# Optimization experiments

Measured on AMD Instinct MI355X. Metric: run time of the kernel, lower is better.

Reference implementation:

```python
import jax, jax.numpy as jnp
import numpy as np

D_MODEL = 1536
BLOCK = 3
N_BLOCKS = D_MODEL // BLOCK
BATCH = 8192
EPS = 1e-8


def setup_inputs() -> dict:
    key = jax.random.key(0)
    ks = jax.random.split(key, 6)
    s = 1.0 / np.sqrt(D_MODEL)  # torch Linear default-ish scale
    x = jax.random.normal(ks[0], (BATCH, D_MODEL), dtype=jnp.float32)
    h_prev = jax.random.normal(ks[1], (BATCH, D_MODEL), dtype=jnp.float32)
    W_biv = jax.random.normal(ks[2], (D_MODEL, D_MODEL), dtype=jnp.float32) * s
    b_biv = jnp.zeros((D_MODEL,), dtype=jnp.float32)  # init.zeros_
    W_dec = jax.random.normal(ks[3], (1, D_MODEL), dtype=jnp.float32) * s
    b_dec = jnp.full((1,), 1.4, dtype=jnp.float32)  # init.constant_(1.4)
    W_in = jax.random.normal(ks[4], (D_MODEL, D_MODEL), dtype=jnp.float32) * s
    b_in = jax.random.normal(ks[5], (D_MODEL,), dtype=jnp.float32) * s
    return {"x": x, "h_prev": h_prev, "W_biv": W_biv, "b_biv": b_biv,
            "W_dec": W_dec, "b_dec": b_dec, "W_in": W_in, "b_in": b_in}


def _quat_rotate_blocks(h_blocks, bivectors):
    # h_blocks, bivectors: (batch, n_blocks, 3)
    norm_b = jnp.maximum(jnp.linalg.norm(bivectors, axis=-1, keepdims=True), EPS)
    half_angle = norm_b / 2
    w = jnp.cos(half_angle)[..., 0]
    s = (jnp.sin(half_angle) / norm_b)[..., 0]  # sin_ha_over_norm[..., 0]
    # NOTE: faithful to source — qx/qy/qz all use component 0 of sin_ha_over_norm
    qx = s * bivectors[..., 2]
    qy = -s * bivectors[..., 1]
    qz = s * bivectors[..., 0]
    vx, vy, vz = h_blocks[..., 0], h_blocks[..., 1], h_blocks[..., 2]
    tx = 2 * (qy * vz - qz * vy)
    ty = 2 * (qz * vx - qx * vz)
    tz = 2 * (qx * vy - qy * vx)
    rx = vx + w * tx + (qy * tz - qz * ty)
    ry = vy + w * ty + (qz * tx - qx * tz)
    rz = vz + w * tz + (qx * ty - qy * tx)
    return jnp.stack([rx, ry, rz], axis=-1)


def reference(x, h_prev, W_biv, b_biv, W_dec, b_dec, W_in, b_in):
    batch = x.shape[0]
    bivectors = (x @ W_biv.T + b_biv).reshape(batch, N_BLOCKS, 3)
    decay = jax.nn.sigmoid(x @ W_dec.T + b_dec)          # (batch, 1)
    injection = x @ W_in.T + b_in                        # (batch, d_model)
    h_blocks = h_prev.reshape(batch, N_BLOCKS, 3)
    rotated = _quat_rotate_blocks(h_blocks, bivectors)
    return decay * rotated.reshape(batch, D_MODEL) + injection
```

## Files before the change

kernel.cpp:

```cpp
#include <hip/hip_runtime.h>
#include <cstdint>

#define D_MODEL 1536
#define BATCH   8192
#define EPS     1e-8f

#define BM 128
#define BN 96
#define BK 32
#define NT (D_MODEL / BK)
#define NTN (D_MODEL / BN)
#define NTM (BATCH / BM)
#define BUF 20480

typedef __attribute__((ext_vector_type(8))) short bf16x8;
typedef __attribute__((ext_vector_type(8))) unsigned short ushort8;
typedef __attribute__((ext_vector_type(4))) float f32x4;

__device__ __forceinline__ unsigned short f2bf(float f) {
  unsigned u = __builtin_bit_cast(unsigned, f);
  u += 0x7fffu + ((u >> 16) & 1u);
  return (unsigned short)(u >> 16);
}

__device__ __forceinline__ ushort8 pack8u(float4 a, float4 b) {
  ushort8 o;
  o[0] = f2bf(a.x); o[1] = f2bf(a.y); o[2] = f2bf(a.z); o[3] = f2bf(a.w);
  o[4] = f2bf(b.x); o[5] = f2bf(b.y); o[6] = f2bf(b.z); o[7] = f2bf(b.w);
  return o;
}

__device__ __forceinline__ void full_drain() {
  asm volatile("s_waitcnt vmcnt(0) lgkmcnt(0)" ::: "memory");
}
__device__ __forceinline__ void vm_drain() {
  asm volatile("s_waitcnt vmcnt(0)" ::: "memory");
}
__device__ __forceinline__ void lgkm_drain() {
  asm volatile("s_waitcnt lgkmcnt(0)" ::: "memory");
}

__device__ __forceinline__ void load_lds16(const void* g, void* l) {
  __builtin_amdgcn_global_load_lds(
      (const __attribute__((address_space(1))) unsigned int*)g,
      (__attribute__((address_space(3))) unsigned int*)l,
      16, 0, 0);
}

__global__ void prep_all(const float* __restrict__ x,
                         const float* __restrict__ wdec,
                         const float* __restrict__ bdec,
                         const float* __restrict__ wbiv,
                         const float* __restrict__ win,
                         unsigned short* __restrict__ xb,
                         unsigned short* __restrict__ wb,
                         float* __restrict__ decay) {
  const int b = blockIdx.x;
  if (b < 2048) {
    int row  = (int)((b * 256 + threadIdx.x) >> 6);
    int lane = threadIdx.x & 63;
    const float4* xr = (const float4*)(x + (long)row * D_MODEL);
    const float4* wr = (const float4*)wdec;
    unsigned short* xo = xb + (long)row * D_MODEL;
    float acc = 0.f;
#pragma unroll
    for (int i = 0; i < 6; ++i) {
      float4 a = xr[lane + 64 * i];
      float4 w = wr[lane + 64 * i];
      acc += a.x * w.x + a.y * w.y + a.z * w.z + a.w * w.w;
      ushort4 o;
      o.x = f2bf(a.x); o.y = f2bf(a.y); o.z = f2bf(a.z); o.w = f2bf(a.w);
      *(ushort4*)(xo + (lane + 64 * i) * 4) = o;
    }
    for (int off = 32; off; off >>= 1) acc += __shfl_xor(acc, off);
    if (lane == 0) decay[row] = 1.f / (1.f + expf(-(acc + bdec[0])));
  } else {
    const long NW4 = (long)D_MODEL * D_MODEL / 4;
    for (long i = (long)(b - 2048) * 256 + threadIdx.x; i < 2 * NW4;
         i += (long)1024 * 256) {
      const float4* src = (i < NW4) ? (const float4*)wbiv : (const float4*)win;
      long j = (i < NW4) ? i : (i - NW4);
      float4 v = src[j];
      ushort4 o;
      o.x = f2bf(v.x); o.y = f2bf(v.y); o.z = f2bf(v.z); o.w = f2bf(v.w);
      *(ushort4*)(wb + 4 * i) = o;
    }
  }
}

__global__ __launch_bounds__(512, 2)
void fused_main(const unsigned short* __restrict__ xb,
                const unsigned short* __restrict__ wb,
                const float* __restrict__ hprev,
                const float* __restrict__ decay,
                const float* __restrict__ bbiv,
                const float* __restrict__ bin,
                float* __restrict__ out) {
  __shared__ __align__(16) char smem[49664];
  float* sBv = (float*)smem;

  const int bid = blockIdx.x;
  const int tm = bid / NTN, tn = bid % NTN;
  const int m0 = tm * BM, n0 = tn * BN;
  const int tid  = threadIdx.x;
  const int lane = tid & 63, wid = tid >> 6;
  const int wr = wid >> 1, wc = wid & 1;
  const int lr = lane & 15;
  const int lk = lane >> 4;

  const unsigned short *gA, *gB1, *gB2;
  int dA, dB1, dB2;
  {
    int f, row, c, cs;
    f = tid;  row = f >> 2; c = f & 3; cs = c ^ ((row >> 1) & 3);
    gA = xb + (long)(m0 + row) * D_MODEL + cs * 8;
    dA = (wid * 64) << 4;
    row = f >> 2; c = f & 3; cs = c ^ ((row >> 1) & 3);
    gB1 = wb + (long)(n0 + row) * D_MODEL + cs * 8;
    gB2 = gB1 + (long)D_MODEL * D_MODEL;
    dB1 = 8192 + ((wid * 64) << 4);
    dB2 = dB1 + 6144;
  }

  auto STAGE = [&](int bb) {
    load_lds16(gA, smem + bb + dA);
    if (tid < 384) {
      load_lds16(gB1, smem + bb + dB1);
      load_lds16(gB2, smem + bb + dB2);
    }
    gA += BK; gB1 += BK; gB2 += BK;
  };

  f32x4 accB[2][3], accI[2][3];
#pragma unroll
  for (int a = 0; a < 2; ++a)
#pragma unroll
    for (int b = 0; b < 3; ++b) { accB[a][b] = (f32x4)0.f; accI[a][b] = (f32x4)0.f; }

  STAGE(0);
  vm_drain();
  __syncthreads();

  for (int t = 0; t < NT; ++t) {
    const int cur = (t & 1) * BUF;
    if (t + 1 < NT) STAGE(((t + 1) & 1) * BUF);

    const unsigned short* cA  = (const unsigned short*)(smem + cur);
    const unsigned short* cB1 = (const unsigned short*)(smem + cur + 8192);
    const unsigned short* cB2 = (const unsigned short*)(smem + cur + 14336);

    {
      bf16x8 a[2], b1[3], b2[3];
#pragma unroll
      for (int mi = 0; mi < 2; ++mi) {
        int R = wr * 32 + mi * 16 + lr;
        a[mi] = *(const bf16x8*)(cA + R * 32 + (lk ^ ((R >> 1) & 3)) * 8);
      }
#pragma unroll
      for (int ni = 0; ni < 3; ++ni) {
        int R = wc * 48 + ni * 16 + lr;
        b1[ni] = *(const bf16x8*)(cB1 + R * 32 + (lk ^ ((R >> 1) & 3)) * 8);
        b2[ni] = *(const bf16x8*)(cB2 + R * 32 + (lk ^ ((R >> 1) & 3)) * 8);
      }
      lgkm_drain();
      __builtin_amdgcn_sched_barrier(0);
#pragma unroll
      for (int mi = 0; mi < 2; ++mi)
#pragma unroll
        for (int ni = 0; ni < 3; ++ni)
          accB[mi][ni] = __builtin_amdgcn_mfma_f32_16x16x32_bf16(
              a[mi], b1[ni], accB[mi][ni], 0, 0, 0);
      __builtin_amdgcn_sched_barrier(0);
#pragma unroll
      for (int mi = 0; mi < 2; ++mi)
#pragma unroll
        for (int ni = 0; ni < 3; ++ni)
          accI[mi][ni] = __builtin_amdgcn_mfma_f32_16x16x32_bf16(
              a[mi], b2[ni], accI[mi][ni], 0, 0, 0);
      __builtin_amdgcn_sched_barrier(0);
    }

    vm_drain();
    __syncthreads();
  }

#pragma unroll
  for (int mi = 0; mi < 2; ++mi)
#pragma unroll
    for (int ni = 0; ni < 3; ++ni) {
      int col = wc * 48 + ni * 16 + lr;
      float bb = bbiv[n0 + col];
#pragma unroll
      for (int r = 0; r < 4; ++r) {
        int row = wr * 32 + mi * 16 + lk * 4 + r;
        sBv[row * 97 + col] = accB[mi][ni][r] + bb;
      }
    }
  full_drain();
  __syncthreads();

#pragma unroll
  for (int mi = 0; mi < 2; ++mi)
#pragma unroll
    for (int ni = 0; ni < 3; ++ni) {
      int col  = wc * 48 + ni * 16 + lr;
      int gcol = n0 + col;
      int c    = (col % 3);
      int lc0  = col - c;
      float binv = bin[gcol];
#pragma unroll
      for (int r = 0; r < 4; ++r) {
        int row  = wr * 32 + mi * 16 + lk * 4 + r;
        int grow = m0 + row;
        float bx = sBv[row * 97 + lc0];
        float by = sBv[row * 97 + lc0 + 1];
        float bz = sBv[row * 97 + lc0 + 2];
        const float* hp = hprev + (long)grow * D_MODEL + (n0 + lc0);
        float vx = hp[0], vy = hp[1], vz = hp[2];
        float nb = sqrtf(bx * bx + by * by + bz * bz);
        nb = fmaxf(nb, EPS);
        float ha = 0.5f * nb;
        float w  = cosf(ha);
        float s  = sinf(ha) / nb;
        float qx = s * bz, qy = -s * by, qz = s * bx;
        float tx = 2.f * (qy * vz - qz * vy);
        float ty = 2.f * (qz * vx - qx * vz);
        float tz = 2.f * (qx * vy - qy * vx);
        float rx = vx + w * tx + (qy * tz - qz * ty);
        float ry = vy + w * ty + (qz * tx - qx * tz);
        float rz = vz + w * tz + (qx * ty - qy * tx);
        float rc = (c == 0) ? rx : ((c == 1) ? ry : rz);
        out[(long)grow * D_MODEL + gcol] =
            decay[grow] * rc + (accI[mi][ni][r] + binv);
      }
    }
}

__global__ __launch_bounds__(256, 2)
void fused_mfma3(const float* __restrict__ x,
                 const float* __restrict__ wbiv,
                 const float* __restrict__ win,
                 const float* __restrict__ hprev,
                 const float* __restrict__ wdec,
                 const float* __restrict__ bdec,
                 const float* __restrict__ bbiv,
                 const float* __restrict__ bin,
                 float* __restrict__ out) {
  __shared__ __align__(16) char smem[50688];
  __shared__ float sDecay[BM];
  unsigned short* sA  = (unsigned short*)smem;
  unsigned short* sB1 = (unsigned short*)(smem + 16384);
  unsigned short* sB2 = (unsigned short*)(smem + 28672);
  float* sBv = (float*)smem;

  const int bid = blockIdx.x;
  const int tm = bid / NTN, tn = bid % NTN;
  const int m0 = tm * BM, n0 = tn * BN;
  const int tid  = threadIdx.x;
  const int lane = tid & 63, wid = tid >> 6;
  const int wr = wid >> 1, wc = wid & 1;
  const int lr = lane & 15;
  const int lk = lane >> 4;

  {
    const float bd = bdec[0];
    const float4* wd4 = (const float4*)wdec;
    for (int rr = 0; rr < 32; ++rr) {
      int row = wid * 32 + rr;
      const float4* xr = (const float4*)(x + (long)(m0 + row) * D_MODEL);
      float acc = 0.f;
#pragma unroll
      for (int i = 0; i < 6; ++i) {
        float4 a = xr[lane + 64 * i];
        float4 b = wd4[lane + 64 * i];
        acc += a.x * b.x + a.y * b.y + a.z * b.z + a.w * b.w;
      }
      for (int off = 32; off; off >>= 1) acc += __shfl_xor(acc, off);
      if (lane == 0) sDecay[row] = 1.f / (1.f + expf(-(acc + bd)));
    }
  }

  f32x4 accB[4][3], accI[4][3];
#pragma unroll
  for (int a = 0; a < 4; ++a)
#pragma unroll
    for (int b = 0; b < 3; ++b) { accB[a][b] = (f32x4)0.f; accI[a][b] = (f32x4)0.f; }

  for (int kt = 0; kt < D_MODEL; kt += 64) {
    full_drain();
    __syncthreads();
#pragma unroll
    for (int i = 0; i < 4; ++i) {
      int f = i * 256 + tid;
      int row = f >> 3, c = f & 7;
      const float4* p = (const float4*)(x + (long)(m0 + row) * D_MODEL + kt + c * 8);
      *(ushort8*)(sA + row * 64 + c * 8) = pack8u(p[0], p[1]);
    }
#pragma unroll
    for (int i = 0; i < 6; ++i) {
      int mat = (i >= 3);
      int g = (i - 3 * mat) * 256 + tid;
      int row = g >> 3, c = g & 7;
      const float* wsrc = mat ? win : wbiv;
      const float4* p = (const float4*)(wsrc + (long)(n0 + row) * D_MODEL + kt + c * 8);
      *(ushort8*)((mat ? sB2 : sB1) + row * 64 + c * 8) = pack8u(p[0], p[1]);
    }
    full_drain();
    __syncthreads();

#pragma unroll
    for (int ks = 0; ks < 2; ++ks) {
      const int k0 = ks * 32 + lk * 8;
      bf16x8 a[4], b1[3], b2[3];
#pragma unroll
      for (int mi = 0; mi < 4; ++mi)
        a[mi] = *(const bf16x8*)(sA + (wr * 64 + mi * 16 + lr) * 64 + k0);
#pragma unroll
      for (int ni = 0; ni < 3; ++ni) {
        b1[ni] = *(const bf16x8*)(sB1 + (wc * 48 + ni * 16 + lr) * 64 + k0);
        b2[ni] = *(const bf16x8*)(sB2 + (wc * 48 + ni * 16 + lr) * 64 + k0);
      }
      full_drain();
      __builtin_amdgcn_sched_barrier(0);
#pragma unroll
      for (int mi = 0; mi < 4; ++mi)
#pragma unroll
        for (int ni = 0; ni < 3; ++ni)
          accB[mi][ni] = __builtin_amdgcn_mfma_f32_16x16x32_bf16(
              a[mi], b1[ni], accB[mi][ni], 0, 0, 0);
      __builtin_amdgcn_sched_barrier(0);
#pragma unroll
      for (int mi = 0; mi < 4; ++mi)
#pragma unroll
        for (int ni = 0; ni < 3; ++ni)
          accI[mi][ni] = __builtin_amdgcn_mfma_f32_16x16x32_bf16(
              a[mi], b2[ni], accI[mi][ni], 0, 0, 0);
      __builtin_amdgcn_sched_barrier(0);
    }
  }

  full_drain();
  __syncthreads();
#pragma unroll
  for (int mi = 0; mi < 4; ++mi)
#pragma unroll
    for (int ni = 0; ni < 3; ++ni) {
      int col = wc * 48 + ni * 16 + lr;
      float bb = bbiv[n0 + col];
#pragma unroll
      for (int r = 0; r < 4; ++r) {
        int row = wr * 64 + mi * 16 + lk * 4 + r;
        sBv[row * 97 + col] = accB[mi][ni][r] + bb;
      }
    }
  full_drain();
  __syncthreads();

#pragma unroll
  for (int mi = 0; mi < 4; ++mi)
#pragma unroll
    for (int ni = 0; ni < 3; ++ni) {
      int col  = wc * 48 + ni * 16 + lr;
      int gcol = n0 + col;
      int c    = (col % 3);
      int lc0  = col - c;
      float binv = bin[gcol];
#pragma unroll
      for (int r = 0; r < 4; ++r) {
        int row  = wr * 64 + mi * 16 + lk * 4 + r;
        int grow = m0 + row;
        float bx = sBv[row * 97 + lc0];
        float by = sBv[row * 97 + lc0 + 1];
        float bz = sBv[row * 97 + lc0 + 2];
        const float* hp = hprev + (long)grow * D_MODEL + (n0 + lc0);
        float vx = hp[0], vy = hp[1], vz = hp[2];
        float nb = sqrtf(bx * bx + by * by + bz * bz);
        nb = fmaxf(nb, EPS);
        float ha = 0.5f * nb;
        float w  = cosf(ha);
        float s  = sinf(ha) / nb;
        float qx = s * bz, qy = -s * by, qz = s * bx;
        float tx = 2.f * (qy * vz - qz * vy);
        float ty = 2.f * (qz * vx - qx * vz);
        float tz = 2.f * (qx * vy - qy * vx);
        float rx = vx + w * tx + (qy * tz - qz * ty);
        float ry = vy + w * ty + (qz * tx - qx * tz);
        float rz = vz + w * tz + (qx * ty - qy * tx);
        float rc = (c == 0) ? rx : ((c == 1) ? ry : rz);
        out[(long)grow * D_MODEL + gcol] =
            sDecay[row] * rc + (accI[mi][ni][r] + binv);
      }
    }
}

extern "C" void kernel_launch(void* const* d_in, const int* in_sizes, int n_in,
                              void* d_out, int out_size, void* d_ws, size_t ws_size,
                              hipStream_t stream) {
  const float* x     = (const float*)d_in[0];
  const float* hprev = (const float*)d_in[1];
  const float* wbiv  = (const float*)d_in[2];
  const float* bbiv  = (const float*)d_in[3];
  const float* wdec  = (const float*)d_in[4];
  const float* bdec  = (const float*)d_in[5];
  const float* win   = (const float*)d_in[6];
  const float* bin   = (const float*)d_in[7];
  float* out = (float*)d_out;

  const size_t XB_B  = 25165824;
  const size_t WB_B  = 9437184;
  const size_t DC_B  = 32768;

  if (ws_size >= XB_B + WB_B + DC_B) {
    char* ws = (char*)d_ws;
    unsigned short* xb = (unsigned short*)ws;
    unsigned short* wb = (unsigned short*)(ws + XB_B);
    float* decay       = (float*)(ws + XB_B + WB_B);
    prep_all<<<dim3(3072), dim3(256), 0, stream>>>(
        x, wdec, bdec, wbiv, win, xb, wb, decay);
    fused_main<<<dim3(NTM * NTN), dim3(512), 0, stream>>>(
        xb, wb, hprev, decay, bbiv, bin, out);
  } else {
    fused_mfma3<<<dim3(NTM * NTN), dim3(256), 0, stream>>>(
        x, wbiv, win, hprev, wdec, bdec, bbiv, bin, out);
  }
}
```

Before: 134.7 us.

## Double K-tile depth to 64 with 8-way swizzle and use fast sin/cos

Raises the K tile from 32 to 64, so the main loop runs half as many iterations and pays half as many barriers and waits on the global-to-LDS staging. Shared memory per buffer doubles to 40 KB, which can cap occupancy at the declared two blocks of 512 threads. Staging is now a uniform unrolled loop of five async loads per thread with precomputed LDS offsets, using an 8-slot XOR swizzle in place of the old 4-slot one. The epilogue also switches sinf/cosf to the hardware __sinf/__cosf intrinsics, trading some accuracy for fewer instructions.

After: 113.5 us. 1.19x faster.

```diff
diff --git a/kernel.cpp b/kernel.cpp
--- a/kernel.cpp
+++ b/kernel.cpp
@@ -7,11 +7,11 @@
 
 #define BM 128
 #define BN 96
-#define BK 32
+#define BK 64
 #define NT (D_MODEL / BK)
 #define NTN (D_MODEL / BN)
 #define NTM (BATCH / BM)
-#define BUF 20480
+#define BUF 40960
 
 typedef __attribute__((ext_vector_type(8))) short bf16x8;
 typedef __attribute__((ext_vector_type(8))) unsigned short ushort8;
@@ -96,7 +96,7 @@
                 const float* __restrict__ bbiv,
                 const float* __restrict__ bin,
                 float* __restrict__ out) {
-  __shared__ __align__(16) char smem[49664];
+  __shared__ __align__(16) char smem[2 * BUF];
   float* sBv = (float*)smem;
 
   const int bid = blockIdx.x;
@@ -108,28 +108,53 @@
   const int lr = lane & 15;
   const int lk = lane >> 4;
 
-  const unsigned short *gA, *gB1, *gB2;
-  int dA, dB1, dB2;
-  {
-    int f, row, c, cs;
-    f = tid;  row = f >> 2; c = f & 3; cs = c ^ ((row >> 1) & 3);
-    gA = xb + (long)(m0 + row) * D_MODEL + cs * 8;
-    dA = (wid * 64) << 4;
-    row = f >> 2; c = f & 3; cs = c ^ ((row >> 1) & 3);
-    gB1 = wb + (long)(n0 + row) * D_MODEL + cs * 8;
-    gB2 = gB1 + (long)D_MODEL * D_MODEL;
-    dB1 = 8192 + ((wid * 64) << 4);
-    dB2 = dB1 + 6144;
+  const unsigned short* gptr[5];
+  int doff[5];
+#pragma unroll
+  for (int i = 0; i < 5; ++i) {
+    int f = i * 512 + tid;
+    if (f < 1024) {
+      int row = f >> 3, c = f & 7, cs = c ^ (row & 7);
+      gptr[i] = xb + (long)(m0 + row) * D_MODEL + cs * 8;
+      doff[i] = f << 4;
+    } else if (f < 1792) {
+      int g = f - 1024;
+      int row = g >> 3, c = g & 7, cs = c ^ (row & 7);
+      gptr[i] = wb + (long)(n0 + row) * D_MODEL + cs * 8;
+      doff[i] = 16384 + (g << 4);
+    } else {
+      int g = f - 1792;
+      int row = g >> 3, c = g & 7, cs = c ^ (row & 7);
+      gptr[i] = wb + (long)D_MODEL * D_MODEL + (long)(n0 + row) * D_MODEL + cs * 8;
+      doff[i] = 28672 + (g << 4);
+    }
   }
 
   auto STAGE = [&](int bb) {
-    load_lds16(gA, smem + bb + dA);
-    if (tid < 384) {
-      load_lds16(gB1, smem + bb + dB1);
-      load_lds16(gB2, smem + bb + dB2);
-    }
-    gA += BK; gB1 += BK; gB2 += BK;
+#pragma unroll
+    for (int i = 0; i < 5; ++i) {
+      load_lds16(gptr[i], smem + bb + doff[i]);
+      gptr[i] += BK;
+    }
   };
+
+  int offA[2][2], offB1[3][2], offB2[3][2];
+#pragma unroll
+  for (int ks = 0; ks < 2; ++ks) {
+    const int slot = ks * 4 + lk;
+#pragma unroll
+    for (int mi = 0; mi < 2; ++mi) {
+      int R = wr * 32 + mi * 16 + lr;
+      offA[mi][ks] = (R * 64 + (slot ^ (R & 7)) * 8) * 2;
+    }
+#pragma unroll
+    for (int ni = 0; ni < 3; ++ni) {
+      int R = wc * 48 + ni * 16 + lr;
+      int o = (R * 64 + (slot ^ (R & 7)) * 8) * 2;
+      offB1[ni][ks] = 16384 + o;
+      offB2[ni][ks] = 28672 + o;
+    }
+  }
 
   f32x4 accB[2][3], accI[2][3];
 #pragma unroll
@@ -145,22 +170,16 @@
     const int cur = (t & 1) * BUF;
     if (t + 1 < NT) STAGE(((t + 1) & 1) * BUF);
 
-    const unsigned short* cA  = (const unsigned short*)(smem + cur);
-    const unsigned short* cB1 = (const unsigned short*)(smem + cur + 8192);
-    const unsigned short* cB2 = (const unsigned short*)(smem + cur + 14336);
-
-    {
+#pragma unroll
+    for (int ks = 0; ks < 2; ++ks) {
       bf16x8 a[2], b1[3], b2[3];
 #pragma unroll
-      for (int mi = 0; mi < 2; ++mi) {
-        int R = wr * 32 + mi * 16 + lr;
-        a[mi] = *(const bf16x8*)(cA + R * 32 + (lk ^ ((R >> 1) & 3)) * 8);
-      }
+      for (int mi = 0; mi < 2; ++mi)
+        a[mi] = *(const bf16x8*)(smem + cur + offA[mi][ks]);
 #pragma unroll
       for (int ni = 0; ni < 3; ++ni) {
-        int R = wc * 48 + ni * 16 + lr;
-        b1[ni] = *(const bf16x8*)(cB1 + R * 32 + (lk ^ ((R >> 1) & 3)) * 8);
-        b2[ni] = *(const bf16x8*)(cB2 + R * 32 + (lk ^ ((R >> 1) & 3)) * 8);
+        b1[ni] = *(const bf16x8*)(smem + cur + offB1[ni][ks]);
+        b2[ni] = *(const bf16x8*)(smem + cur + offB2[ni][ks]);
       }
       lgkm_drain();
       __builtin_amdgcn_sched_barrier(0);
@@ -220,8 +239,8 @@
         float nb = sqrtf(bx * bx + by * by + bz * bz);
         nb = fmaxf(nb, EPS);
         float ha = 0.5f * nb;
-        float w  = cosf(ha);
-        float s  = sinf(ha) / nb;
+        float w  = __cosf(ha);
+        float s  = __sinf(ha) / nb;
         float qx = s * bz, qy = -s * by, qz = s * bx;
         float tx = 2.f * (qy * vz - qz * vy);
         float ty = 2.f * (qz * vx - qx * vz);
```
